# Kernel optimization log

Measured on AMD Instinct MI355X. Metric: run time of the kernel, lower is better.

## Reference

```python
import jax, jax.numpy as jnp
import numpy as np

N, E = 50000, 1600000
F_IN, EDGE_DIM, HID, HEADS, NCLS = 64, 16, 128, 4, 40
C = HID // HEADS  # per-head dim = 32


def setup_inputs() -> dict:
    key = jax.random.key(0)
    ks = jax.random.split(key, 20)
    s = 0.1
    inp = {
        'x': jax.random.normal(ks[0], (N, F_IN), jnp.float32),
        'edge_index': jax.random.randint(ks[1], (2, E), 0, N, jnp.int64),
        'edge_attr': jax.random.normal(ks[2], (E, EDGE_DIM), jnp.float32),
        # layer 1 params
        'W1': jax.random.normal(ks[3], (HID, F_IN), jnp.float32) * s,
        'as1': jax.random.normal(ks[4], (HEADS, C), jnp.float32) * s,
        'ad1': jax.random.normal(ks[5], (HEADS, C), jnp.float32) * s,
        'ae1': jax.random.normal(ks[6], (HEADS, C), jnp.float32) * s,
        'We1': jax.random.normal(ks[7], (HID, EDGE_DIM), jnp.float32) * s,
        'b1': jnp.zeros((HID,), jnp.float32),
        # layer 2 params
        'W2': jax.random.normal(ks[8], (HID, HID), jnp.float32) * s,
        'as2': jax.random.normal(ks[9], (HEADS, C), jnp.float32) * s,
        'ad2': jax.random.normal(ks[10], (HEADS, C), jnp.float32) * s,
        'ae2': jax.random.normal(ks[11], (HEADS, C), jnp.float32) * s,
        'We2': jax.random.normal(ks[12], (HID, EDGE_DIM), jnp.float32) * s,
        'b2': jnp.zeros((HID,), jnp.float32),
        # final classifier
        'Wlin': jax.random.normal(ks[13], (NCLS, HID), jnp.float32) * s,
        'blin': jnp.zeros((NCLS,), jnp.float32),
    }
    return inp


def gat_conv(x, src, dst, eattr, W, a_s, a_d, a_e, We, b):
    """PyG GATConv (concat=True, add_self_loops=True, fill_value='mean'), eval mode."""
    n = x.shape[0]
    H, Cd = a_s.shape
    h = (x @ W.T).reshape(n, H, Cd)  # [N,H,C]
    # self-loop edge_attr = per-destination mean of incoming edge_attr
    cnt = jax.ops.segment_sum(jnp.ones((dst.shape[0],), eattr.dtype), dst, num_segments=n)
    mean_ea = jax.ops.segment_sum(eattr, dst, num_segments=n) / jnp.maximum(cnt, 1.0)[:, None]
    loops = jnp.arange(n, dtype=src.dtype)
    s_idx = jnp.concatenate([src, loops])
    d_idx = jnp.concatenate([dst, loops])
    ea = jnp.concatenate([eattr, mean_ea], axis=0)  # [E+N, edge_dim]
    e = (ea @ We.T).reshape(-1, H, Cd)
    # edge-wise attention logits
    alpha = (h * a_s).sum(-1)[s_idx] + (h * a_d).sum(-1)[d_idx] + (e * a_e).sum(-1)  # [E+N,H]
    alpha = jax.nn.leaky_relu(alpha, 0.2)
    # segment softmax over destination neighborhoods (every node has a self-loop)
    amax = jax.ops.segment_max(alpha, d_idx, num_segments=n)
    ex = jnp.exp(alpha - amax[d_idx])
    den = jax.ops.segment_sum(ex, d_idx, num_segments=n)
    coef = ex / (den[d_idx] + 1e-16)
    out = jax.ops.segment_sum(h[s_idx] * coef[:, :, None], d_idx, num_segments=n)
    return out.reshape(n, H * Cd) + b


def reference(x, edge_index, edge_attr, W1, as1, ad1, ae1, We1, b1,
              W2, as2, ad2, ae2, We2, b2, Wlin, blin):
    src, dst = edge_index[0], edge_index[1]
    h = jax.nn.relu(gat_conv(x, src, dst, edge_attr, W1, as1, ad1, ae1, We1, b1))
    h = jax.nn.relu(gat_conv(h, src, dst, edge_attr, W2, as2, ad2, ae2, We2, b2))
    logits = h @ Wlin.T + blin
    return jax.nn.log_softmax(logits, axis=1)
```

## Files before the change

kernel.cpp:

```cpp
#include <hip/hip_runtime.h>
#include <hip/hip_bf16.h>
#include <math.h>


#define CHUNK 2048
#define CAPC 4608

typedef __attribute__((ext_vector_type(8))) short short8;
typedef __attribute__((ext_vector_type(4))) float floatx4;

__device__ __forceinline__ unsigned short f2bf(float f) {
  unsigned u = __float_as_uint(f);
  unsigned r = u + 0x7FFFu + ((u >> 16) & 1u);
  return (unsigned short)(r >> 16);
}
__device__ __forceinline__ float bf2f(unsigned short b) {
  return __uint_as_float(((unsigned)b) << 16);
}

__global__ __launch_bounds__(512) void hist_kernel(const int* __restrict__ dst,
                                                   int* __restrict__ bucketCnt,
                                                   int E, int NB) {
  __shared__ int hist[512];
  const int tid = threadIdx.x;
  hist[tid] = 0;
  __syncthreads();
  const int e0 = blockIdx.x * CHUNK, e1 = min(e0 + CHUNK, E);
  for (int e = e0 + tid; e < e1; e += 512) atomicAdd(&hist[dst[e] >> 7], 1);
  __syncthreads();
  if (tid < NB && hist[tid]) atomicAdd(&bucketCnt[tid], hist[tid]);
}

__global__ __launch_bounds__(512) void scanB_kernel(const int* __restrict__ bucketCnt,
                                                    int* __restrict__ bucketOffs,
                                                    int* __restrict__ bucketPos,
                                                    int* __restrict__ offs,
                                                    int NB, int N, int E) {
  __shared__ int sc[512];
  const int tid = threadIdx.x;
  const int v = (tid < NB) ? bucketCnt[tid] : 0;
  sc[tid] = v;
  __syncthreads();
  for (int off = 1; off < 512; off <<= 1) {
    int t = (tid >= off) ? sc[tid - off] : 0;
    __syncthreads();
    sc[tid] += t;
    __syncthreads();
  }
  const int excl = sc[tid] - v;
  if (tid < NB) { bucketOffs[tid] = excl; bucketPos[tid] = excl; }
  if (tid == 0) { bucketOffs[NB] = E; offs[N] = E; }
}

__global__ __launch_bounds__(512) void partB_kernel(const int* __restrict__ src,
                                                    const int* __restrict__ dst,
                                                    int* __restrict__ bucketPos,
                                                    int2* __restrict__ binned,
                                                    int E, int NB) {
  __shared__ int hist[512], sc[512], lbase[513], gbase[512], lcnt[512];
  __shared__ int2 stage[CHUNK];
  const int tid = threadIdx.x;
  const int e0 = blockIdx.x * CHUNK;
  const int e1 = min(e0 + CHUNK, E);
  hist[tid] = 0; lcnt[tid] = 0;
  __syncthreads();
  for (int e = e0 + tid; e < e1; e += 512) atomicAdd(&hist[dst[e] >> 7], 1);
  __syncthreads();
  sc[tid] = hist[tid];
  __syncthreads();
  for (int off = 1; off < 512; off <<= 1) {
    int t = (tid >= off) ? sc[tid - off] : 0;
    __syncthreads();
    sc[tid] += t;
    __syncthreads();
  }
  lbase[tid + 1] = sc[tid];
  if (tid == 0) lbase[0] = 0;
  if (tid < NB && hist[tid] > 0) gbase[tid] = atomicAdd(&bucketPos[tid], hist[tid]);
  __syncthreads();
  for (int e = e0 + tid; e < e1; e += 512) {
    const int d = dst[e];
    const int b = d >> 7;
    const int lr = atomicAdd(&lcnt[b], 1);
    int2 v;
    v.x = src[e];
    v.y = (int)(((unsigned)(d & 127) << 25) | (unsigned)e);
    stage[lbase[b] + lr] = v;
  }
  __syncthreads();
  const int total = e1 - e0;
  for (int t = tid; t < total; t += 512) {
    int lo = 0, hi = 511;
    while (lo < hi) {
      int mid = (lo + hi + 1) >> 1;
      if (lbase[mid] <= t) lo = mid; else hi = mid - 1;
    }
    binned[gbase[lo] + (t - lbase[lo])] = stage[t];
  }
}

__global__ __launch_bounds__(256) void passC_kernel(const int2* __restrict__ binned,
                                                    const int* __restrict__ bucketOffs,
                                                    int* __restrict__ srcS,
                                                    int* __restrict__ elist,
                                                    int* __restrict__ offs, int N) {
  __shared__ int cnt[128], dbase[129], dpos[128];
  __shared__ int2 stage[CAPC];
  const int tid = threadIdx.x;
  const int b = blockIdx.x;
  const int bo = bucketOffs[b], be = bucketOffs[b + 1];
  const int m = be - bo;
  if (tid < 128) { cnt[tid] = 0; dpos[tid] = 0; }
  __syncthreads();
  for (int t = tid; t < m; t += 256) {
    int2 v = binned[bo + t];
    if (t < CAPC) stage[t] = v;
    atomicAdd(&cnt[((unsigned)v.y) >> 25], 1);
  }
  __syncthreads();
  for (int off = 1; off < 128; off <<= 1) {
    int t = (tid < 128 && tid >= (unsigned)off) ? cnt[tid - off] : 0;
    __syncthreads();
    if (tid < 128) cnt[tid] += t;
    __syncthreads();
  }
  if (tid == 0) dbase[0] = 0;
  if (tid < 128) dbase[tid + 1] = cnt[tid];
  __syncthreads();
  const int dcnt = min(128, N - (b << 7));
  if (tid < dcnt) offs[(b << 7) + tid] = bo + dbase[tid];
  for (int t = tid; t < m; t += 256) {
    int2 v = (t < CAPC) ? stage[t] : binned[bo + t];
    const unsigned py = (unsigned)v.y;
    const int dl = py >> 25;
    const int p = dbase[dl] + atomicAdd(&dpos[dl], 1);
    srcS[bo + p] = v.x;
    elist[bo + p] = (int)(py & 0x1FFFFFFu);
  }
}

__global__ __launch_bounds__(128) void wa_kernel(const float* __restrict__ ae1,
                                                 const float* __restrict__ We1,
                                                 const float* __restrict__ ae2,
                                                 const float* __restrict__ We2,
                                                 float* __restrict__ Wa) {
  int t = threadIdx.x;
  const float* ae = (t < 64) ? ae1 : ae2;
  const float* We = (t < 64) ? We1 : We2;
  int h = (t >> 4) & 3;
  int d = t & 15;
  float s = 0.f;
  for (int c = 0; c < 32; ++c) s += ae[h * 32 + c] * We[(h * 32 + c) * 16 + d];
  Wa[t] = s;
}

__global__ __launch_bounds__(256) void cvt3_kernel(const float* __restrict__ a,
                                                   unsigned short* __restrict__ ao, int na,
                                                   const float* __restrict__ b,
                                                   unsigned short* __restrict__ bo, int nb,
                                                   const float* __restrict__ c,
                                                   unsigned short* __restrict__ co, int nc) {
  int i = blockIdx.x * 256 + threadIdx.x;
  if (i < na) ao[i] = f2bf(a[i]);
  else if (i < na + nb) bo[i - na] = f2bf(b[i - na]);
  else if (i < na + nb + nc) co[i - na - nb] = f2bf(c[i - na - nb]);
}

__global__ __launch_bounds__(256) void cvtw_kernel(const float* __restrict__ Wlin,
                                                   unsigned short* __restrict__ whi,
                                                   unsigned short* __restrict__ wlo) {
  int i = blockIdx.x * 256 + threadIdx.x;
  if (i >= 48 * 128) return;
  float v = (i < 40 * 128) ? Wlin[i] : 0.f;
  unsigned short h = f2bf(v);
  whi[i] = h;
  wlo[i] = f2bf(v - bf2f(h));
}

__global__ __launch_bounds__(256) void alphae12_kernel(const int* __restrict__ elist,
                                                       const float* __restrict__ ea,
                                                       const float* __restrict__ Wa,
                                                       unsigned short* __restrict__ ae1s,
                                                       unsigned short* __restrict__ ae2s,
                                                       int E) {
  __shared__ float wa[128];
  if (threadIdx.x < 128) wa[threadIdx.x] = Wa[threadIdx.x];
  __syncthreads();
  int j = blockIdx.x * 256 + threadIdx.x;
  if (j >= E) return;
  const int e = elist[j];
  const float4* p = (const float4*)(ea + (size_t)e * 16);
  float4 q0 = p[0], q1 = p[1], q2 = p[2], q3 = p[3];
  float v[16] = {q0.x, q0.y, q0.z, q0.w, q1.x, q1.y, q1.z, q1.w,
                 q2.x, q2.y, q2.z, q2.w, q3.x, q3.y, q3.z, q3.w};
  unsigned short rr[8];
#pragma unroll
  for (int h = 0; h < 8; ++h) {
    float s = 0.f;
#pragma unroll
    for (int d = 0; d < 16; ++d) s += v[d] * wa[h * 16 + d];
    rr[h] = f2bf(s);
  }
  ushort4 lo; lo.x = rr[0]; lo.y = rr[1]; lo.z = rr[2]; lo.w = rr[3];
  ushort4 hi; hi.x = rr[4]; hi.y = rr[5]; hi.z = rr[6]; hi.w = rr[7];
  *(ushort4*)(ae1s + (size_t)j * 4) = lo;
  *(ushort4*)(ae2s + (size_t)j * 4) = hi;
}

__global__ __launch_bounds__(256) void gemm_mfma_kernel(const unsigned short* __restrict__ X,
                                                        const unsigned short* __restrict__ Wb,
                                                        unsigned short* __restrict__ H,
                                                        int n, int K) {
  const int w = threadIdx.x >> 6;
  const int lane = threadIdx.x & 63;
  const int m0 = blockIdx.x * 64;
  const int quad = lane >> 4;
  const int l15 = lane & 15;
  floatx4 acc[4][2];
#pragma unroll
  for (int mt = 0; mt < 4; ++mt)
#pragma unroll
    for (int nt = 0; nt < 2; ++nt) acc[mt][nt] = (floatx4)(0.f);

  int rowm[4];
#pragma unroll
  for (int mt = 0; mt < 4; ++mt) {
    int r = m0 + mt * 16 + l15;
    rowm[mt] = (r < n) ? r : (n - 1);
  }
  const int ncol0 = (w << 5) + l15;

  for (int kc = 0; kc < K; kc += 32) {
    const int koff = kc + (quad << 3);
    short8 a[4], b[2];
#pragma unroll
    for (int mt = 0; mt < 4; ++mt)
      a[mt] = *(const short8*)(X + (size_t)rowm[mt] * K + koff);
#pragma unroll
    for (int nt = 0; nt < 2; ++nt)
      b[nt] = *(const short8*)(Wb + (size_t)(ncol0 + nt * 16) * K + koff);
#pragma unroll
    for (int mt = 0; mt < 4; ++mt)
#pragma unroll
      for (int nt = 0; nt < 2; ++nt)
        acc[mt][nt] = __builtin_amdgcn_mfma_f32_16x16x32_bf16(a[mt], b[nt], acc[mt][nt], 0, 0, 0);
  }
#pragma unroll
  for (int mt = 0; mt < 4; ++mt) {
    const int rbase = m0 + mt * 16 + (quad << 2);
#pragma unroll
    for (int nt = 0; nt < 2; ++nt) {
      const int col = ncol0 + nt * 16;
#pragma unroll
      for (int r = 0; r < 4; ++r) {
        const int row = rbase + r;
        if (row < n) H[(size_t)row * 128 + col] = f2bf(acc[mt][nt][r]);
      }
    }
  }
}

__global__ __launch_bounds__(256) void score_kernel(const unsigned short* __restrict__ h,
                                                    const float* __restrict__ a_s,
                                                    const float* __restrict__ a_d,
                                                    float* __restrict__ ssc,
                                                    float* __restrict__ dsc, int n) {
  int gid = blockIdx.x * 256 + threadIdx.x;
  int node = gid >> 6;
  int lane = threadIdx.x & 63;
  if (node >= n) return;
  int ch = lane * 2;
  ushort2 hq = *(const ushort2*)(h + (size_t)node * 128 + ch);
  float h0 = bf2f(hq.x), h1 = bf2f(hq.y);
  float ps = h0 * a_s[ch] + h1 * a_s[ch + 1];
  float pd = h0 * a_d[ch] + h1 * a_d[ch + 1];
#pragma unroll
  for (int off = 8; off; off >>= 1) {
    ps += __shfl_xor(ps, off, 16);
    pd += __shfl_xor(pd, off, 16);
  }
  if ((lane & 15) == 0) {
    int head = lane >> 4;
    ssc[node * 4 + head] = ps;
    dsc[node * 4 + head] = pd;
  }
}

__device__ __forceinline__ float leaky02(float a) { return a > 0.f ? a : 0.2f * a; }
__device__ __forceinline__ float sel4(float4 v, int h) {
  return (h == 0) ? v.x : (h == 1) ? v.y : (h == 2) ? v.z : v.w;
}

__global__ __launch_bounds__(256) void agg_kernel(const unsigned short* __restrict__ hin,
                                                  const float* __restrict__ ssc,
                                                  const float* __restrict__ dsc,
                                                  const unsigned short* __restrict__ aeS,
                                                  const int* __restrict__ offs,
                                                  const int* __restrict__ srcS,
                                                  const float* __restrict__ bias,
                                                  unsigned short* __restrict__ hout, int n) {
  __shared__ int sbuf[4][64];
  __shared__ float pbuf[4][256];
  const int tid = threadIdx.x;
  const int wv = tid >> 6;
  const int lane = tid & 63;
  const int node = blockIdx.x * 4 + wv;
  if (node >= n) return;
  const int l32 = lane & 31;
  const int half = lane >> 5;
  const int ch4 = l32 * 4;
  const int headB = l32 >> 3;
  const float4 dv = *(const float4*)(dsc + (size_t)node * 4);
  float4 l4 = make_float4(0.f, 0.f, 0.f, 0.f);
  float4 sa = make_float4(0.f, 0.f, 0.f, 0.f);
  float acc[4] = {0.f, 0.f, 0.f, 0.f};
  const int j0 = offs[node], j1 = offs[node + 1];

  for (int jc = j0; jc < j1; jc += 64) {
    const int len = min(64, j1 - jc);
    float4 p4 = make_float4(0.f, 0.f, 0.f, 0.f);
    int sv = 0;
    if (lane < len) {
      const int j = jc + lane;
      sv = srcS[j];
      const ushort4 aq = *(const ushort4*)(aeS + (size_t)j * 4);
      const float4 ae4 = make_float4(bf2f(aq.x), bf2f(aq.y), bf2f(aq.z), bf2f(aq.w));
      const float4 ss4 = *(const float4*)(ssc + (size_t)sv * 4);
      sa.x += ae4.x; sa.y += ae4.y; sa.z += ae4.z; sa.w += ae4.w;
      p4.x = __expf(leaky02(ss4.x + dv.x + ae4.x));
      p4.y = __expf(leaky02(ss4.y + dv.y + ae4.y));
      p4.z = __expf(leaky02(ss4.z + dv.z + ae4.z));
      p4.w = __expf(leaky02(ss4.w + dv.w + ae4.w));
    }
    sbuf[wv][lane] = sv;
    *(float4*)(&pbuf[wv][lane * 4]) = p4;
    l4.x += p4.x; l4.y += p4.y; l4.z += p4.z; l4.w += p4.w;
    int k = 0;
    for (; k + 8 <= len; k += 8) {
      int kk0 = k + half, kk1 = k + 2 + half, kk2 = k + 4 + half, kk3 = k + 6 + half;
      int s0 = sbuf[wv][kk0], s1 = sbuf[wv][kk1], s2 = sbuf[wv][kk2], s3 = sbuf[wv][kk3];
      float p0 = pbuf[wv][kk0 * 4 + headB], p1 = pbuf[wv][kk1 * 4 + headB];
      float p2 = pbuf[wv][kk2 * 4 + headB], p3 = pbuf[wv][kk3 * 4 + headB];
      uint2 d0 = *(const uint2*)(hin + (size_t)s0 * 128 + ch4);
      uint2 d1 = *(const uint2*)(hin + (size_t)s1 * 128 + ch4);
      uint2 d2 = *(const uint2*)(hin + (size_t)s2 * 128 + ch4);
      uint2 d3 = *(const uint2*)(hin + (size_t)s3 * 128 + ch4);
      acc[0] += p0 * __uint_as_float(d0.x << 16);
      acc[1] += p0 * __uint_as_float(d0.x & 0xFFFF0000u);
      acc[2] += p0 * __uint_as_float(d0.y << 16);
      acc[3] += p0 * __uint_as_float(d0.y & 0xFFFF0000u);
      acc[0] += p1 * __uint_as_float(d1.x << 16);
      acc[1] += p1 * __uint_as_float(d1.x & 0xFFFF0000u);
      acc[2] += p1 * __uint_as_float(d1.y << 16);
      acc[3] += p1 * __uint_as_float(d1.y & 0xFFFF0000u);
      acc[0] += p2 * __uint_as_float(d2.x << 16);
      acc[1] += p2 * __uint_as_float(d2.x & 0xFFFF0000u);
      acc[2] += p2 * __uint_as_float(d2.y << 16);
      acc[3] += p2 * __uint_as_float(d2.y & 0xFFFF0000u);
      acc[0] += p3 * __uint_as_float(d3.x << 16);
      acc[1] += p3 * __uint_as_float(d3.x & 0xFFFF0000u);
      acc[2] += p3 * __uint_as_float(d3.y << 16);
      acc[3] += p3 * __uint_as_float(d3.y & 0xFFFF0000u);
    }
    for (; k < len; k += 2) {
      int kk = k + half;
      if (kk < len) {
        int s = sbuf[wv][kk];
        float p = pbuf[wv][kk * 4 + headB];
        uint2 d = *(const uint2*)(hin + (size_t)s * 128 + ch4);
        acc[0] += p * __uint_as_float(d.x << 16);
        acc[1] += p * __uint_as_float(d.x & 0xFFFF0000u);
        acc[2] += p * __uint_as_float(d.y << 16);
        acc[3] += p * __uint_as_float(d.y & 0xFFFF0000u);
      }
    }
  }

#pragma unroll
  for (int off = 32; off; off >>= 1) {
    sa.x += __shfl_xor(sa.x, off);
    sa.y += __shfl_xor(sa.y, off);
    sa.z += __shfl_xor(sa.z, off);
    sa.w += __shfl_xor(sa.w, off);
    l4.x += __shfl_xor(l4.x, off);
    l4.y += __shfl_xor(l4.y, off);
    l4.z += __shfl_xor(l4.z, off);
    l4.w += __shfl_xor(l4.w, off);
  }
#pragma unroll
  for (int i = 0; i < 4; ++i) acc[i] += __shfl_xor(acc[i], 32);

  const int deg = j1 - j0;
  const float invd = 1.f / fmaxf((float)deg, 1.f);
  const float ssn = ssc[(size_t)node * 4 + headB];
  const float aloop = leaky02(ssn + sel4(dv, headB) + sel4(sa, headB) * invd);
  const float pl = __expf(aloop);
  const float lF = sel4(l4, headB) + pl;
  const uint2 hd = *(const uint2*)(hin + (size_t)node * 128 + ch4);
  const float hv0 = __uint_as_float(hd.x << 16);
  const float hv1 = __uint_as_float(hd.x & 0xFFFF0000u);
  const float hv2 = __uint_as_float(hd.y << 16);
  const float hv3 = __uint_as_float(hd.y & 0xFFFF0000u);
  const float inv = 1.f / (lF + 1e-16f);
  const float4 bi = *(const float4*)(bias + ch4);
  const float o0 = fmaxf((acc[0] + pl * hv0) * inv + bi.x, 0.f);
  const float o1 = fmaxf((acc[1] + pl * hv1) * inv + bi.y, 0.f);
  const float o2 = fmaxf((acc[2] + pl * hv2) * inv + bi.z, 0.f);
  const float o3 = fmaxf((acc[3] + pl * hv3) * inv + bi.w, 0.f);
  if (half == 0) {
    ushort4 o;
    o.x = f2bf(o0); o.y = f2bf(o1); o.z = f2bf(o2); o.w = f2bf(o3);
    *(ushort4*)(hout + (size_t)node * 128 + ch4) = o;
  }
}

__global__ __launch_bounds__(256) void classifier_kernel(const unsigned short* __restrict__ h,
                                                         const unsigned short* __restrict__ Whi,
                                                         const unsigned short* __restrict__ Wlo,
                                                         const float* __restrict__ blin,
                                                         float* __restrict__ out, int n) {
  const int w = threadIdx.x >> 6;
  const int lane = threadIdx.x & 63;
  const int quad = lane >> 4;
  const int l15 = lane & 15;
  const int row0 = blockIdx.x * 64 + w * 16;
  if (row0 >= n) return;
  int rowm = row0 + l15;
  if (rowm >= n) rowm = n - 1;
  floatx4 acc[3];
#pragma unroll
  for (int nt = 0; nt < 3; ++nt) acc[nt] = (floatx4)(0.f);
  const size_t hbase = (size_t)rowm * 128;
#pragma unroll
  for (int kc = 0; kc < 128; kc += 32) {
    const int koff = kc + (quad << 3);
    short8 a = *(const short8*)(h + hbase + koff);
#pragma unroll
    for (int nt = 0; nt < 3; ++nt) {
      short8 bh = *(const short8*)(Whi + (size_t)(nt * 16 + l15) * 128 + koff);
      short8 bl = *(const short8*)(Wlo + (size_t)(nt * 16 + l15) * 128 + koff);
      acc[nt] = __builtin_amdgcn_mfma_f32_16x16x32_bf16(a, bh, acc[nt], 0, 0, 0);
      acc[nt] = __builtin_amdgcn_mfma_f32_16x16x32_bf16(a, bl, acc[nt], 0, 0, 0);
    }
  }
  const float bl0 = blin[l15];
  const float bl1 = blin[16 + l15];
  const float bl2 = (l15 < 8) ? blin[32 + l15] : 0.f;
#pragma unroll
  for (int r = 0; r < 4; ++r) {
    const int rrow = row0 + (quad << 2) + r;
    const float v0 = acc[0][r] + bl0;
    const float v1 = acc[1][r] + bl1;
    const float v2 = (l15 < 8) ? (acc[2][r] + bl2) : -INFINITY;
    float m = fmaxf(v0, fmaxf(v1, v2));
#pragma unroll
    for (int off = 8; off; off >>= 1) m = fmaxf(m, __shfl_xor(m, off, 16));
    const float e2 = (l15 < 8) ? __expf(v2 - m) : 0.f;
    float s = __expf(v0 - m) + __expf(v1 - m) + e2;
#pragma unroll
    for (int off = 8; off; off >>= 1) s += __shfl_xor(s, off, 16);
    const float ls = m + __logf(s);
    if (rrow < n) {
      float* po = out + (size_t)rrow * 40;
      po[l15] = v0 - ls;
      po[16 + l15] = v1 - ls;
      if (l15 < 8) po[32 + l15] = v2 - ls;
    }
  }
}

extern "C" void kernel_launch(void* const* d_in, const int* in_sizes, int n_in,
                              void* d_out, int out_size, void* d_ws, size_t ws_size,
                              hipStream_t stream) {
  const float* x    = (const float*)d_in[0];
  const int*   eidx = (const int*)d_in[1];
  const float* ea   = (const float*)d_in[2];
  const float* W1   = (const float*)d_in[3];
  const float* as1  = (const float*)d_in[4];
  const float* ad1  = (const float*)d_in[5];
  const float* ae1w = (const float*)d_in[6];
  const float* We1  = (const float*)d_in[7];
  const float* b1   = (const float*)d_in[8];
  const float* W2   = (const float*)d_in[9];
  const float* as2  = (const float*)d_in[10];
  const float* ad2  = (const float*)d_in[11];
  const float* ae2w = (const float*)d_in[12];
  const float* We2  = (const float*)d_in[13];
  const float* b2   = (const float*)d_in[14];
  const float* Wlin = (const float*)d_in[15];
  const float* blin = (const float*)d_in[16];
  float* out = (float*)d_out;

  const int N = in_sizes[0] / 64;
  const int E = in_sizes[1] / 2;
  const int* src = eidx;
  const int* dst = eidx + E;
  const int NB = (N + 127) >> 7;

  char* wsb = (char*)d_ws;
  size_t off = 0;
  auto alloc = [&](size_t bytes) -> void* {
    void* p = wsb + off;
    off = (off + bytes + 255) & ~(size_t)255;
    return p;
  };
  int* bucketCnt  = (int*)alloc(512 * 4);
  int* bucketOffs = (int*)alloc(513 * 4);
  int* bucketPos  = (int*)alloc(512 * 4);
  int* offs       = (int*)alloc((size_t)(N + 1) * 4);
  void* bhA       = alloc((size_t)E * 8 > (size_t)N * 256 ? (size_t)E * 8 : (size_t)N * 256);
  int2* binned    = (int2*)bhA;
  unsigned short* hA = (unsigned short*)bhA;
  int* srcS       = (int*)alloc((size_t)E * 4);
  int* elist      = (int*)alloc((size_t)E * 4);
  float* Wa       = (float*)alloc(128 * 4);
  unsigned short* xb  = (unsigned short*)alloc((size_t)N * 64 * 2);
  unsigned short* Wb1 = (unsigned short*)alloc(128 * 64 * 2);
  unsigned short* Wb2 = (unsigned short*)alloc(128 * 128 * 2);
  unsigned short* Wlh = (unsigned short*)alloc(48 * 128 * 2);
  unsigned short* Wll = (unsigned short*)alloc(48 * 128 * 2);
  float* ssc      = (float*)alloc((size_t)N * 4 * 4);
  float* dsc      = (float*)alloc((size_t)N * 4 * 4);
  unsigned short* ae1s = (unsigned short*)alloc((size_t)E * 4 * 2);
  unsigned short* ae2s = (unsigned short*)alloc((size_t)E * 4 * 2);
  unsigned short* hB   = (unsigned short*)alloc((size_t)N * 128 * 2);

  const int ge = (E + 255) / 256;
  const int gg = (N + 63) / 64;
  const int gs = (N + 3) / 4;
  const int gp = (E + CHUNK - 1) / CHUNK;
  const int ncvt = N * 64 + 128 * 64 + 128 * 128;

  hipMemsetAsync(bucketCnt, 0, 512 * 4, stream);
  hist_kernel<<<gp, 512, 0, stream>>>(dst, bucketCnt, E, NB);
  scanB_kernel<<<1, 512, 0, stream>>>(bucketCnt, bucketOffs, bucketPos, offs, NB, N, E);
  partB_kernel<<<gp, 512, 0, stream>>>(src, dst, bucketPos, binned, E, NB);
  passC_kernel<<<NB, 256, 0, stream>>>(binned, bucketOffs, srcS, elist, offs, N);

  wa_kernel<<<1, 128, 0, stream>>>(ae1w, We1, ae2w, We2, Wa);
  cvt3_kernel<<<(ncvt + 255) / 256, 256, 0, stream>>>(x, xb, N * 64, W1, Wb1, 128 * 64,
                                                      W2, Wb2, 128 * 128);
  cvtw_kernel<<<24, 256, 0, stream>>>(Wlin, Wlh, Wll);
  alphae12_kernel<<<ge, 256, 0, stream>>>(elist, ea, Wa, ae1s, ae2s, E);

  gemm_mfma_kernel<<<gg, 256, 0, stream>>>(xb, Wb1, hA, N, 64);
  score_kernel<<<gs, 256, 0, stream>>>(hA, as1, ad1, ssc, dsc, N);
  agg_kernel<<<gs, 256, 0, stream>>>(hA, ssc, dsc, ae1s, offs, srcS, b1, hB, N);

  gemm_mfma_kernel<<<gg, 256, 0, stream>>>(hB, Wb2, hA, N, 128);
  score_kernel<<<gs, 256, 0, stream>>>(hA, as2, ad2, ssc, dsc, N);
  agg_kernel<<<gs, 256, 0, stream>>>(hA, ssc, dsc, ae2s, offs, srcS, b2, hB, N);

  classifier_kernel<<<gg, 256, 0, stream>>>(hB, Wlh, Wll, blin, out, N);
}
```

Baseline: 478.9 us.

## Replace two-pass bucket partition CSR build with atomic count-scan-scatter

Swaps the bucketed two-level partition sort (hist, bucket scan, partB, passC) for a per-node degree count with global atomics, a three-stage prefix scan, and an atomic-cursor scatter into CSR order. The edge-attention precompute now reads edge attributes sequentially and scatters its bf16 outputs to each edge's CSR position, rather than gathering through an edge list. This removes the staging buffers and binary searches but relies on heavy global atomics on random destinations. Order within each neighbourhood becomes nondeterministic, which may slightly change summation order and locality.

```diff
diff --git a/kernel.cpp b/kernel.cpp
--- a/kernel.cpp
+++ b/kernel.cpp
@@ -2,9 +2,6 @@
 #include <hip/hip_bf16.h>
 #include <math.h>
 
-
-#define CHUNK 2048
-#define CAPC 4608
 
 typedef __attribute__((ext_vector_type(8))) short short8;
 typedef __attribute__((ext_vector_type(4))) float floatx4;
@@ -18,125 +15,70 @@
   return __uint_as_float(((unsigned)b) << 16);
 }
 
-__global__ __launch_bounds__(512) void hist_kernel(const int* __restrict__ dst,
-                                                   int* __restrict__ bucketCnt,
-                                                   int E, int NB) {
-  __shared__ int hist[512];
+
+__global__ __launch_bounds__(256) void countN_kernel(const int* __restrict__ dst,
+                                                     int* __restrict__ cnt, int E) {
+  int i = blockIdx.x * 256 + threadIdx.x;
+  const int stride = gridDim.x * 256;
+  for (; i < E; i += stride) atomicAdd(&cnt[dst[i]], 1);
+}
+
+__global__ __launch_bounds__(256) void scanA_kernel(const int* __restrict__ cnt,
+                                                    int* __restrict__ offs,
+                                                    int* __restrict__ blockSum, int N) {
+  __shared__ int sc[256];
   const int tid = threadIdx.x;
-  hist[tid] = 0;
-  __syncthreads();
-  const int e0 = blockIdx.x * CHUNK, e1 = min(e0 + CHUNK, E);
-  for (int e = e0 + tid; e < e1; e += 512) atomicAdd(&hist[dst[e] >> 7], 1);
-  __syncthreads();
-  if (tid < NB && hist[tid]) atomicAdd(&bucketCnt[tid], hist[tid]);
-}
-
-__global__ __launch_bounds__(512) void scanB_kernel(const int* __restrict__ bucketCnt,
-                                                    int* __restrict__ bucketOffs,
-                                                    int* __restrict__ bucketPos,
-                                                    int* __restrict__ offs,
-                                                    int NB, int N, int E) {
-  __shared__ int sc[512];
-  const int tid = threadIdx.x;
-  const int v = (tid < NB) ? bucketCnt[tid] : 0;
+  const int i = blockIdx.x * 256 + tid;
+  const int v = (i < N) ? cnt[i] : 0;
   sc[tid] = v;
   __syncthreads();
-  for (int off = 1; off < 512; off <<= 1) {
+  for (int off = 1; off < 256; off <<= 1) {
     int t = (tid >= off) ? sc[tid - off] : 0;
     __syncthreads();
     sc[tid] += t;
     __syncthreads();
   }
-  const int excl = sc[tid] - v;
-  if (tid < NB) { bucketOffs[tid] = excl; bucketPos[tid] = excl; }
-  if (tid == 0) { bucketOffs[NB] = E; offs[N] = E; }
-}
-
-__global__ __launch_bounds__(512) void partB_kernel(const int* __restrict__ src,
-                                                    const int* __restrict__ dst,
-                                                    int* __restrict__ bucketPos,
-                                                    int2* __restrict__ binned,
-                                                    int E, int NB) {
-  __shared__ int hist[512], sc[512], lbase[513], gbase[512], lcnt[512];
-  __shared__ int2 stage[CHUNK];
+  if (i < N) offs[i] = sc[tid] - v;
+  if (tid == 255) blockSum[blockIdx.x] = sc[255];
+}
+
+__global__ __launch_bounds__(256) void scanBlk_kernel(int* __restrict__ blockSum, int NBLK) {
+  __shared__ int sc[256];
   const int tid = threadIdx.x;
-  const int e0 = blockIdx.x * CHUNK;
-  const int e1 = min(e0 + CHUNK, E);
-  hist[tid] = 0; lcnt[tid] = 0;
+  const int v = (tid < NBLK) ? blockSum[tid] : 0;
+  sc[tid] = v;
   __syncthreads();
-  for (int e = e0 + tid; e < e1; e += 512) atomicAdd(&hist[dst[e] >> 7], 1);
-  __syncthreads();
-  sc[tid] = hist[tid];
-  __syncthreads();
-  for (int off = 1; off < 512; off <<= 1) {
+  for (int off = 1; off < 256; off <<= 1) {
     int t = (tid >= off) ? sc[tid - off] : 0;
     __syncthreads();
     sc[tid] += t;
     __syncthreads();
   }
-  lbase[tid + 1] = sc[tid];
-  if (tid == 0) lbase[0] = 0;
-  if (tid < NB && hist[tid] > 0) gbase[tid] = atomicAdd(&bucketPos[tid], hist[tid]);
-  __syncthreads();
-  for (int e = e0 + tid; e < e1; e += 512) {
-    const int d = dst[e];
-    const int b = d >> 7;
-    const int lr = atomicAdd(&lcnt[b], 1);
-    int2 v;
-    v.x = src[e];
-    v.y = (int)(((unsigned)(d & 127) << 25) | (unsigned)e);
-    stage[lbase[b] + lr] = v;
-  }
-  __syncthreads();
-  const int total = e1 - e0;
-  for (int t = tid; t < total; t += 512) {
-    int lo = 0, hi = 511;
-    while (lo < hi) {
-      int mid = (lo + hi + 1) >> 1;
-      if (lbase[mid] <= t) lo = mid; else hi = mid - 1;
-    }
-    binned[gbase[lo] + (t - lbase[lo])] = stage[t];
-  }
-}
-
-__global__ __launch_bounds__(256) void passC_kernel(const int2* __restrict__ binned,
-                                                    const int* __restrict__ bucketOffs,
-                                                    int* __restrict__ srcS,
-                                                    int* __restrict__ elist,
-                                                    int* __restrict__ offs, int N) {
-  __shared__ int cnt[128], dbase[129], dpos[128];
-  __shared__ int2 stage[CAPC];
-  const int tid = threadIdx.x;
-  const int b = blockIdx.x;
-  const int bo = bucketOffs[b], be = bucketOffs[b + 1];
-  const int m = be - bo;
-  if (tid < 128) { cnt[tid] = 0; dpos[tid] = 0; }
-  __syncthreads();
-  for (int t = tid; t < m; t += 256) {
-    int2 v = binned[bo + t];
-    if (t < CAPC) stage[t] = v;
-    atomicAdd(&cnt[((unsigned)v.y) >> 25], 1);
-  }
-  __syncthreads();
-  for (int off = 1; off < 128; off <<= 1) {
-    int t = (tid < 128 && tid >= (unsigned)off) ? cnt[tid - off] : 0;
-    __syncthreads();
-    if (tid < 128) cnt[tid] += t;
-    __syncthreads();
-  }
-  if (tid == 0) dbase[0] = 0;
-  if (tid < 128) dbase[tid + 1] = cnt[tid];
-  __syncthreads();
-  const int dcnt = min(128, N - (b << 7));
-  if (tid < dcnt) offs[(b << 7) + tid] = bo + dbase[tid];
-  for (int t = tid; t < m; t += 256) {
-    int2 v = (t < CAPC) ? stage[t] : binned[bo + t];
-    const unsigned py = (unsigned)v.y;
-    const int dl = py >> 25;
-    const int p = dbase[dl] + atomicAdd(&dpos[dl], 1);
-    srcS[bo + p] = v.x;
-    elist[bo + p] = (int)(py & 0x1FFFFFFu);
-  }
+  if (tid < NBLK) blockSum[tid] = sc[tid] - v;
+}
+
+__global__ __launch_bounds__(256) void finz_kernel(int* __restrict__ offs,
+                                                   const int* __restrict__ blockSum,
+                                                   int* __restrict__ cursor, int N, int E) {
+  const int i = blockIdx.x * 256 + threadIdx.x;
+  if (i < N) {
+    const int v = offs[i] + blockSum[i >> 8];
+    offs[i] = v;
+    cursor[i] = v;
+  }
+  if (i == N) offs[N] = E;
+}
+
+__global__ __launch_bounds__(256) void scatter_kernel(const int* __restrict__ src,
+                                                      const int* __restrict__ dst,
+                                                      int* __restrict__ cursor,
+                                                      int* __restrict__ srcS,
+                                                      int* __restrict__ pos, int E) {
+  const int e = blockIdx.x * 256 + threadIdx.x;
+  if (e >= E) return;
+  const int p = atomicAdd(&cursor[dst[e]], 1);
+  srcS[p] = src[e];
+  pos[e] = p;
 }
 
 __global__ __launch_bounds__(128) void wa_kernel(const float* __restrict__ ae1,
@@ -177,7 +119,7 @@
   wlo[i] = f2bf(v - bf2f(h));
 }
 
-__global__ __launch_bounds__(256) void alphae12_kernel(const int* __restrict__ elist,
+__global__ __launch_bounds__(256) void alphae12_kernel(const int* __restrict__ pos,
                                                        const float* __restrict__ ea,
                                                        const float* __restrict__ Wa,
                                                        unsigned short* __restrict__ ae1s,
@@ -186,9 +128,8 @@
   __shared__ float wa[128];
   if (threadIdx.x < 128) wa[threadIdx.x] = Wa[threadIdx.x];
   __syncthreads();
-  int j = blockIdx.x * 256 + threadIdx.x;
-  if (j >= E) return;
-  const int e = elist[j];
+  int e = blockIdx.x * 256 + threadIdx.x;
+  if (e >= E) return;
   const float4* p = (const float4*)(ea + (size_t)e * 16);
   float4 q0 = p[0], q1 = p[1], q2 = p[2], q3 = p[3];
   float v[16] = {q0.x, q0.y, q0.z, q0.w, q1.x, q1.y, q1.z, q1.w,
@@ -203,8 +144,9 @@
   }
   ushort4 lo; lo.x = rr[0]; lo.y = rr[1]; lo.z = rr[2]; lo.w = rr[3];
   ushort4 hi; hi.x = rr[4]; hi.y = rr[5]; hi.z = rr[6]; hi.w = rr[7];
-  *(ushort4*)(ae1s + (size_t)j * 4) = lo;
-  *(ushort4*)(ae2s + (size_t)j * 4) = hi;
+  const int pp = pos[e];
+  *(ushort4*)(ae1s + (size_t)pp * 4) = lo;
+  *(ushort4*)(ae2s + (size_t)pp * 4) = hi;
 }
 
 __global__ __launch_bounds__(256) void gemm_mfma_kernel(const unsigned short* __restrict__ X,
@@ -495,7 +437,6 @@
   const int E = in_sizes[1] / 2;
   const int* src = eidx;
   const int* dst = eidx + E;
-  const int NB = (N + 127) >> 7;
 
   char* wsb = (char*)d_ws;
   size_t off = 0;
@@ -504,15 +445,13 @@
     off = (off + bytes + 255) & ~(size_t)255;
     return p;
   };
-  int* bucketCnt  = (int*)alloc(512 * 4);
-  int* bucketOffs = (int*)alloc(513 * 4);
-  int* bucketPos  = (int*)alloc(512 * 4);
+  int* cnt        = (int*)alloc((size_t)N * 4);
   int* offs       = (int*)alloc((size_t)(N + 1) * 4);
-  void* bhA       = alloc((size_t)E * 8 > (size_t)N * 256 ? (size_t)E * 8 : (size_t)N * 256);
-  int2* binned    = (int2*)bhA;
-  unsigned short* hA = (unsigned short*)bhA;
+  int* cursor     = (int*)alloc((size_t)N * 4);
+  int* blockSum   = (int*)alloc(256 * 4);
+  unsigned short* hA = (unsigned short*)alloc((size_t)N * 256);
   int* srcS       = (int*)alloc((size_t)E * 4);
-  int* elist      = (int*)alloc((size_t)E * 4);
+  int* pos        = (int*)alloc((size_t)E * 4);
   float* Wa       = (float*)alloc(128 * 4);
   unsigned short* xb  = (unsigned short*)alloc((size_t)N * 64 * 2);
   unsigned short* Wb1 = (unsigned short*)alloc(128 * 64 * 2);
@@ -528,20 +467,21 @@
   const int ge = (E + 255) / 256;
   const int gg = (N + 63) / 64;
   const int gs = (N + 3) / 4;
-  const int gp = (E + CHUNK - 1) / CHUNK;
+  const int NBLK = (N + 255) / 256;
   const int ncvt = N * 64 + 128 * 64 + 128 * 128;
 
-  hipMemsetAsync(bucketCnt, 0, 512 * 4, stream);
-  hist_kernel<<<gp, 512, 0, stream>>>(dst, bucketCnt, E, NB);
-  scanB_kernel<<<1, 512, 0, stream>>>(bucketCnt, bucketOffs, bucketPos, offs, NB, N, E);
-  partB_kernel<<<gp, 512, 0, stream>>>(src, dst, bucketPos, binned, E, NB);
-  passC_kernel<<<NB, 256, 0, stream>>>(binned, bucketOffs, srcS, elist, offs, N);
+  hipMemsetAsync(cnt, 0, (size_t)N * 4, stream);
+  countN_kernel<<<2048, 256, 0, stream>>>(dst, cnt, E);
+  scanA_kernel<<<NBLK, 256, 0, stream>>>(cnt, offs, blockSum, N);
+  scanBlk_kernel<<<1, 256, 0, stream>>>(blockSum, NBLK);
+  finz_kernel<<<(N + 256) / 256 + 1, 256, 0, stream>>>(offs, blockSum, cursor, N, E);
+  scatter_kernel<<<ge, 256, 0, stream>>>(src, dst, cursor, srcS, pos, E);
 
   wa_kernel<<<1, 128, 0, stream>>>(ae1w, We1, ae2w, We2, Wa);
   cvt3_kernel<<<(ncvt + 255) / 256, 256, 0, stream>>>(x, xb, N * 64, W1, Wb1, 128 * 64,
                                                       W2, Wb2, 128 * 128);
   cvtw_kernel<<<24, 256, 0, stream>>>(Wlin, Wlh, Wll);
-  alphae12_kernel<<<ge, 256, 0, stream>>>(elist, ea, Wa, ae1s, ae2s, E);
+  alphae12_kernel<<<ge, 256, 0, stream>>>(pos, ea, Wa, ae1s, ae2s, E);
 
   gemm_mfma_kernel<<<gg, 256, 0, stream>>>(xb, Wb1, hA, N, 64);
   score_kernel<<<gs, 256, 0, stream>>>(hA, as1, ad1, ssc, dsc, N);
```

After: 632.8 us. +32.2%, slower.

## Compute edge attention terms in edge order and carry them through the sort

Applied to the files above, without the earlier changes.

Edge-attribute attention projections are now computed in original edge order, so the edge_attr reads are contiguous. The results travel as payload through the two-pass bucket partition, which makes the elist index array and the scattered gather of edge_attr rows unnecessary. Source indices are packed into 16 bits next to the local destination, which assumes N fits in 16 bits. The cost is wider records in the partition passes (20 bytes per edge instead of 8) and extra intermediate traffic, plus aliasing of scratch buffers.

```diff
diff --git a/kernel.cpp b/kernel.cpp
--- a/kernel.cpp
+++ b/kernel.cpp
@@ -4,7 +4,6 @@
 
 
 #define CHUNK 2048
-#define CAPC 4608
 
 typedef __attribute__((ext_vector_type(8))) short short8;
 typedef __attribute__((ext_vector_type(4))) float floatx4;
@@ -16,127 +15,6 @@
 }
 __device__ __forceinline__ float bf2f(unsigned short b) {
   return __uint_as_float(((unsigned)b) << 16);
-}
-
-__global__ __launch_bounds__(512) void hist_kernel(const int* __restrict__ dst,
-                                                   int* __restrict__ bucketCnt,
-                                                   int E, int NB) {
-  __shared__ int hist[512];
-  const int tid = threadIdx.x;
-  hist[tid] = 0;
-  __syncthreads();
-  const int e0 = blockIdx.x * CHUNK, e1 = min(e0 + CHUNK, E);
-  for (int e = e0 + tid; e < e1; e += 512) atomicAdd(&hist[dst[e] >> 7], 1);
-  __syncthreads();
-  if (tid < NB && hist[tid]) atomicAdd(&bucketCnt[tid], hist[tid]);
-}
-
-__global__ __launch_bounds__(512) void scanB_kernel(const int* __restrict__ bucketCnt,
-                                                    int* __restrict__ bucketOffs,
-                                                    int* __restrict__ bucketPos,
-                                                    int* __restrict__ offs,
-                                                    int NB, int N, int E) {
-  __shared__ int sc[512];
-  const int tid = threadIdx.x;
-  const int v = (tid < NB) ? bucketCnt[tid] : 0;
-  sc[tid] = v;
-  __syncthreads();
-  for (int off = 1; off < 512; off <<= 1) {
-    int t = (tid >= off) ? sc[tid - off] : 0;
-    __syncthreads();
-    sc[tid] += t;
-    __syncthreads();
-  }
-  const int excl = sc[tid] - v;
-  if (tid < NB) { bucketOffs[tid] = excl; bucketPos[tid] = excl; }
-  if (tid == 0) { bucketOffs[NB] = E; offs[N] = E; }
-}
-
-__global__ __launch_bounds__(512) void partB_kernel(const int* __restrict__ src,
-                                                    const int* __restrict__ dst,
-                                                    int* __restrict__ bucketPos,
-                                                    int2* __restrict__ binned,
-                                                    int E, int NB) {
-  __shared__ int hist[512], sc[512], lbase[513], gbase[512], lcnt[512];
-  __shared__ int2 stage[CHUNK];
-  const int tid = threadIdx.x;
-  const int e0 = blockIdx.x * CHUNK;
-  const int e1 = min(e0 + CHUNK, E);
-  hist[tid] = 0; lcnt[tid] = 0;
-  __syncthreads();
-  for (int e = e0 + tid; e < e1; e += 512) atomicAdd(&hist[dst[e] >> 7], 1);
-  __syncthreads();
-  sc[tid] = hist[tid];
-  __syncthreads();
-  for (int off = 1; off < 512; off <<= 1) {
-    int t = (tid >= off) ? sc[tid - off] : 0;
-    __syncthreads();
-    sc[tid] += t;
-    __syncthreads();
-  }
-  lbase[tid + 1] = sc[tid];
-  if (tid == 0) lbase[0] = 0;
-  if (tid < NB && hist[tid] > 0) gbase[tid] = atomicAdd(&bucketPos[tid], hist[tid]);
-  __syncthreads();
-  for (int e = e0 + tid; e < e1; e += 512) {
-    const int d = dst[e];
-    const int b = d >> 7;
-    const int lr = atomicAdd(&lcnt[b], 1);
-    int2 v;
-    v.x = src[e];
-    v.y = (int)(((unsigned)(d & 127) << 25) | (unsigned)e);
-    stage[lbase[b] + lr] = v;
-  }
-  __syncthreads();
-  const int total = e1 - e0;
-  for (int t = tid; t < total; t += 512) {
-    int lo = 0, hi = 511;
-    while (lo < hi) {
-      int mid = (lo + hi + 1) >> 1;
-      if (lbase[mid] <= t) lo = mid; else hi = mid - 1;
-    }
-    binned[gbase[lo] + (t - lbase[lo])] = stage[t];
-  }
-}
-
-__global__ __launch_bounds__(256) void passC_kernel(const int2* __restrict__ binned,
-                                                    const int* __restrict__ bucketOffs,
-                                                    int* __restrict__ srcS,
-                                                    int* __restrict__ elist,
-                                                    int* __restrict__ offs, int N) {
-  __shared__ int cnt[128], dbase[129], dpos[128];
-  __shared__ int2 stage[CAPC];
-  const int tid = threadIdx.x;
-  const int b = blockIdx.x;
-  const int bo = bucketOffs[b], be = bucketOffs[b + 1];
-  const int m = be - bo;
-  if (tid < 128) { cnt[tid] = 0; dpos[tid] = 0; }
-  __syncthreads();
-  for (int t = tid; t < m; t += 256) {
-    int2 v = binned[bo + t];
-    if (t < CAPC) stage[t] = v;
-    atomicAdd(&cnt[((unsigned)v.y) >> 25], 1);
-  }
-  __syncthreads();
-  for (int off = 1; off < 128; off <<= 1) {
-    int t = (tid < 128 && tid >= (unsigned)off) ? cnt[tid - off] : 0;
-    __syncthreads();
-    if (tid < 128) cnt[tid] += t;
-    __syncthreads();
-  }
-  if (tid == 0) dbase[0] = 0;
-  if (tid < 128) dbase[tid + 1] = cnt[tid];
-  __syncthreads();
-  const int dcnt = min(128, N - (b << 7));
-  if (tid < dcnt) offs[(b << 7) + tid] = bo + dbase[tid];
-  for (int t = tid; t < m; t += 256) {
-    int2 v = (t < CAPC) ? stage[t] : binned[bo + t];
-    const unsigned py = (unsigned)v.y;
-    const int dl = py >> 25;
-    const int p = dbase[dl] + atomicAdd(&dpos[dl], 1);
-    srcS[bo + p] = v.x;
-    elist[bo + p] = (int)(py & 0x1FFFFFFu);
-  }
 }
 
 __global__ __launch_bounds__(128) void wa_kernel(const float* __restrict__ ae1,
@@ -154,6 +32,170 @@
   Wa[t] = s;
 }
 
+__global__ __launch_bounds__(256) void alphaseq_kernel(const float* __restrict__ ea,
+                                                       const float* __restrict__ Wa,
+                                                       uint2* __restrict__ tA1,
+                                                       uint2* __restrict__ tA2, int E) {
+  __shared__ float wa[128];
+  if (threadIdx.x < 128) wa[threadIdx.x] = Wa[threadIdx.x];
+  __syncthreads();
+  int e = blockIdx.x * 256 + threadIdx.x;
+  if (e >= E) return;
+  const float4* p = (const float4*)(ea + (size_t)e * 16);
+  float4 q0 = p[0], q1 = p[1], q2 = p[2], q3 = p[3];
+  float v[16] = {q0.x, q0.y, q0.z, q0.w, q1.x, q1.y, q1.z, q1.w,
+                 q2.x, q2.y, q2.z, q2.w, q3.x, q3.y, q3.z, q3.w};
+  unsigned short rr[8];
+#pragma unroll
+  for (int h = 0; h < 8; ++h) {
+    float s = 0.f;
+#pragma unroll
+    for (int d = 0; d < 16; ++d) s += v[d] * wa[h * 16 + d];
+    rr[h] = f2bf(s);
+  }
+  uint2 lo, hi;
+  lo.x = ((unsigned)rr[1] << 16) | rr[0];
+  lo.y = ((unsigned)rr[3] << 16) | rr[2];
+  hi.x = ((unsigned)rr[5] << 16) | rr[4];
+  hi.y = ((unsigned)rr[7] << 16) | rr[6];
+  tA1[e] = lo;
+  tA2[e] = hi;
+}
+
+__global__ __launch_bounds__(512) void hist_kernel(const int* __restrict__ dst,
+                                                   int* __restrict__ bucketCnt,
+                                                   int E, int NB) {
+  __shared__ int hist[512];
+  const int tid = threadIdx.x;
+  hist[tid] = 0;
+  __syncthreads();
+  const int e0 = blockIdx.x * CHUNK, e1 = min(e0 + CHUNK, E);
+  for (int e = e0 + tid; e < e1; e += 512) atomicAdd(&hist[dst[e] >> 7], 1);
+  __syncthreads();
+  if (tid < NB && hist[tid]) atomicAdd(&bucketCnt[tid], hist[tid]);
+}
+
+__global__ __launch_bounds__(512) void scanB_kernel(const int* __restrict__ bucketCnt,
+                                                    int* __restrict__ bucketOffs,
+                                                    int* __restrict__ bucketPos,
+                                                    int* __restrict__ offs,
+                                                    int NB, int N, int E) {
+  __shared__ int sc[512];
+  const int tid = threadIdx.x;
+  const int v = (tid < NB) ? bucketCnt[tid] : 0;
+  sc[tid] = v;
+  __syncthreads();
+  for (int off = 1; off < 512; off <<= 1) {
+    int t = (tid >= off) ? sc[tid - off] : 0;
+    __syncthreads();
+    sc[tid] += t;
+    __syncthreads();
+  }
+  const int excl = sc[tid] - v;
+  if (tid < NB) { bucketOffs[tid] = excl; bucketPos[tid] = excl; }
+  if (tid == 0) { bucketOffs[NB] = E; offs[N] = E; }
+}
+
+__global__ __launch_bounds__(512) void partB_kernel(const int* __restrict__ src,
+                                                    const int* __restrict__ dst,
+                                                    const uint2* __restrict__ tA1,
+                                                    const uint2* __restrict__ tA2,
+                                                    int* __restrict__ bucketPos,
+                                                    int4* __restrict__ binned16,
+                                                    int* __restrict__ binned4,
+                                                    int E, int NB) {
+  __shared__ int hist[512], sc[512], lbase[513], gbase[512], lcnt[512];
+  __shared__ int4 stg16[CHUNK];
+  __shared__ int stg4[CHUNK];
+  const int tid = threadIdx.x;
+  const int e0 = blockIdx.x * CHUNK;
+  const int e1 = min(e0 + CHUNK, E);
+  hist[tid] = 0; lcnt[tid] = 0;
+  __syncthreads();
+  for (int e = e0 + tid; e < e1; e += 512) atomicAdd(&hist[dst[e] >> 7], 1);
+  __syncthreads();
+  sc[tid] = hist[tid];
+  __syncthreads();
+  for (int off = 1; off < 512; off <<= 1) {
+    int t = (tid >= off) ? sc[tid - off] : 0;
+    __syncthreads();
+    sc[tid] += t;
+    __syncthreads();
+  }
+  lbase[tid + 1] = sc[tid];
+  if (tid == 0) lbase[0] = 0;
+  if (tid < NB && hist[tid] > 0) gbase[tid] = atomicAdd(&bucketPos[tid], hist[tid]);
+  __syncthreads();
+  for (int e = e0 + tid; e < e1; e += 512) {
+    const int d = dst[e];
+    const int b = d >> 7;
+    const int lr = atomicAdd(&lcnt[b], 1);
+    const uint2 a1 = tA1[e];
+    const uint2 a2 = tA2[e];
+    int4 v;
+    v.x = (src[e] & 0xFFFF) | ((d & 127) << 16);
+    v.y = (int)a1.x;
+    v.z = (int)a1.y;
+    v.w = (int)a2.x;
+    const int sp = lbase[b] + lr;
+    stg16[sp] = v;
+    stg4[sp] = (int)a2.y;
+  }
+  __syncthreads();
+  const int total = e1 - e0;
+  for (int t = tid; t < total; t += 512) {
+    int lo = 0, hi = 511;
+    while (lo < hi) {
+      int mid = (lo + hi + 1) >> 1;
+      if (lbase[mid] <= t) lo = mid; else hi = mid - 1;
+    }
+    const int g = gbase[lo] + (t - lbase[lo]);
+    binned16[g] = stg16[t];
+    binned4[g] = stg4[t];
+  }
+}
+
+__global__ __launch_bounds__(256) void passC_kernel(const int4* __restrict__ binned16,
+                                                    const int* __restrict__ binned4,
+                                                    const int* __restrict__ bucketOffs,
+                                                    int* __restrict__ srcS,
+                                                    uint2* __restrict__ aeS1,
+                                                    uint2* __restrict__ aeS2,
+                                                    int* __restrict__ offs, int N) {
+  __shared__ int cnt[128], dbase[129], dpos[128];
+  const int tid = threadIdx.x;
+  const int b = blockIdx.x;
+  const int bo = bucketOffs[b], be = bucketOffs[b + 1];
+  const int m = be - bo;
+  if (tid < 128) { cnt[tid] = 0; dpos[tid] = 0; }
+  __syncthreads();
+  for (int t = tid; t < m; t += 256) {
+    const int4 v = binned16[bo + t];
+    atomicAdd(&cnt[(v.x >> 16) & 127], 1);
+  }
+  __syncthreads();
+  for (int off = 1; off < 128; off <<= 1) {
+    int t = (tid < 128 && tid >= (unsigned)off) ? cnt[tid - off] : 0;
+    __syncthreads();
+    if (tid < 128) cnt[tid] += t;
+    __syncthreads();
+  }
+  if (tid == 0) dbase[0] = 0;
+  if (tid < 128) dbase[tid + 1] = cnt[tid];
+  __syncthreads();
+  const int dcnt = min(128, N - (b << 7));
+  if (tid < dcnt) offs[(b << 7) + tid] = bo + dbase[tid];
+  for (int t = tid; t < m; t += 256) {
+    const int4 v = binned16[bo + t];
+    const int w4 = binned4[bo + t];
+    const int dl = (v.x >> 16) & 127;
+    const int p = dbase[dl] + atomicAdd(&dpos[dl], 1);
+    srcS[bo + p] = v.x & 0xFFFF;
+    aeS1[bo + p] = make_uint2((unsigned)v.y, (unsigned)v.z);
+    aeS2[bo + p] = make_uint2((unsigned)v.w, (unsigned)w4);
+  }
+}
+
 __global__ __launch_bounds__(256) void cvt3_kernel(const float* __restrict__ a,
                                                    unsigned short* __restrict__ ao, int na,
                                                    const float* __restrict__ b,
@@ -175,36 +217,6 @@
   unsigned short h = f2bf(v);
   whi[i] = h;
   wlo[i] = f2bf(v - bf2f(h));
-}
-
-__global__ __launch_bounds__(256) void alphae12_kernel(const int* __restrict__ elist,
-                                                       const float* __restrict__ ea,
-                                                       const float* __restrict__ Wa,
-                                                       unsigned short* __restrict__ ae1s,
-                                                       unsigned short* __restrict__ ae2s,
-                                                       int E) {
-  __shared__ float wa[128];
-  if (threadIdx.x < 128) wa[threadIdx.x] = Wa[threadIdx.x];
-  __syncthreads();
-  int j = blockIdx.x * 256 + threadIdx.x;
-  if (j >= E) return;
-  const int e = elist[j];
-  const float4* p = (const float4*)(ea + (size_t)e * 16);
-  float4 q0 = p[0], q1 = p[1], q2 = p[2], q3 = p[3];
-  float v[16] = {q0.x, q0.y, q0.z, q0.w, q1.x, q1.y, q1.z, q1.w,
-                 q2.x, q2.y, q2.z, q2.w, q3.x, q3.y, q3.z, q3.w};
-  unsigned short rr[8];
-#pragma unroll
-  for (int h = 0; h < 8; ++h) {
-    float s = 0.f;
-#pragma unroll
-    for (int d = 0; d < 16; ++d) s += v[d] * wa[h * 16 + d];
-    rr[h] = f2bf(s);
-  }
-  ushort4 lo; lo.x = rr[0]; lo.y = rr[1]; lo.z = rr[2]; lo.w = rr[3];
-  ushort4 hi; hi.x = rr[4]; hi.y = rr[5]; hi.z = rr[6]; hi.w = rr[7];
-  *(ushort4*)(ae1s + (size_t)j * 4) = lo;
-  *(ushort4*)(ae2s + (size_t)j * 4) = hi;
 }
 
 __global__ __launch_bounds__(256) void gemm_mfma_kernel(const unsigned short* __restrict__ X,
@@ -508,22 +520,25 @@
   int* bucketOffs = (int*)alloc(513 * 4);
   int* bucketPos  = (int*)alloc(512 * 4);
   int* offs       = (int*)alloc((size_t)(N + 1) * 4);
-  void* bhA       = alloc((size_t)E * 8 > (size_t)N * 256 ? (size_t)E * 8 : (size_t)N * 256);
-  int2* binned    = (int2*)bhA;
-  unsigned short* hA = (unsigned short*)bhA;
+  uint2* tA1      = (uint2*)alloc((size_t)E * 8);
+  uint2* tA2      = (uint2*)alloc((size_t)E * 8);
+  void* regC      = alloc((size_t)E * 16);
+  int4* binned16  = (int4*)regC;
+  unsigned short* hA = (unsigned short*)regC;
+  void* regD      = alloc((size_t)E * 4);
+  int* binned4    = (int*)regD;
+  unsigned short* xb = (unsigned short*)regD;
   int* srcS       = (int*)alloc((size_t)E * 4);
-  int* elist      = (int*)alloc((size_t)E * 4);
   float* Wa       = (float*)alloc(128 * 4);
-  unsigned short* xb  = (unsigned short*)alloc((size_t)N * 64 * 2);
   unsigned short* Wb1 = (unsigned short*)alloc(128 * 64 * 2);
   unsigned short* Wb2 = (unsigned short*)alloc(128 * 128 * 2);
   unsigned short* Wlh = (unsigned short*)alloc(48 * 128 * 2);
   unsigned short* Wll = (unsigned short*)alloc(48 * 128 * 2);
   float* ssc      = (float*)alloc((size_t)N * 4 * 4);
   float* dsc      = (float*)alloc((size_t)N * 4 * 4);
-  unsigned short* ae1s = (unsigned short*)alloc((size_t)E * 4 * 2);
-  unsigned short* ae2s = (unsigned short*)alloc((size_t)E * 4 * 2);
-  unsigned short* hB   = (unsigned short*)alloc((size_t)N * 128 * 2);
+  unsigned short* hB = (unsigned short*)alloc((size_t)N * 128 * 2);
+  uint2* aeS1 = tA1;
+  uint2* aeS2 = tA2;
 
   const int ge = (E + 255) / 256;
   const int gg = (N + 63) / 64;
@@ -532,24 +547,24 @@
   const int ncvt = N * 64 + 128 * 64 + 128 * 128;
 
   hipMemsetAsync(bucketCnt, 0, 512 * 4, stream);
+  wa_kernel<<<1, 128, 0, stream>>>(ae1w, We1, ae2w, We2, Wa);
+  alphaseq_kernel<<<ge, 256, 0, stream>>>(ea, Wa, tA1, tA2, E);
   hist_kernel<<<gp, 512, 0, stream>>>(dst, bucketCnt, E, NB);
   scanB_kernel<<<1, 512, 0, stream>>>(bucketCnt, bucketOffs, bucketPos, offs, NB, N, E);
-  partB_kernel<<<gp, 512, 0, stream>>>(src, dst, bucketPos, binned, E, NB);
-  passC_kernel<<<NB, 256, 0, stream>>>(binned, bucketOffs, srcS, elist, offs, N);
-
-  wa_kernel<<<1, 128, 0, stream>>>(ae1w, We1, ae2w, We2, Wa);
+  partB_kernel<<<gp, 512, 0, stream>>>(src, dst, tA1, tA2, bucketPos, binned16, binned4, E, NB);
+  passC_kernel<<<NB, 256, 0, stream>>>(binned16, binned4, bucketOffs, srcS, aeS1, aeS2, offs, N);
+
   cvt3_kernel<<<(ncvt + 255) / 256, 256, 0, stream>>>(x, xb, N * 64, W1, Wb1, 128 * 64,
                                                       W2, Wb2, 128 * 128);
   cvtw_kernel<<<24, 256, 0, stream>>>(Wlin, Wlh, Wll);
-  alphae12_kernel<<<ge, 256, 0, stream>>>(elist, ea, Wa, ae1s, ae2s, E);
 
   gemm_mfma_kernel<<<gg, 256, 0, stream>>>(xb, Wb1, hA, N, 64);
   score_kernel<<<gs, 256, 0, stream>>>(hA, as1, ad1, ssc, dsc, N);
-  agg_kernel<<<gs, 256, 0, stream>>>(hA, ssc, dsc, ae1s, offs, srcS, b1, hB, N);
+  agg_kernel<<<gs, 256, 0, stream>>>(hA, ssc, dsc, (const unsigned short*)aeS1, offs, srcS, b1, hB, N);
 
   gemm_mfma_kernel<<<gg, 256, 0, stream>>>(hB, Wb2, hA, N, 128);
   score_kernel<<<gs, 256, 0, stream>>>(hA, as2, ad2, ssc, dsc, N);
-  agg_kernel<<<gs, 256, 0, stream>>>(hA, ssc, dsc, ae2s, offs, srcS, b2, hB, N);
+  agg_kernel<<<gs, 256, 0, stream>>>(hA, ssc, dsc, (const unsigned short*)aeS2, offs, srcS, b2, hB, N);
 
   classifier_kernel<<<gg, 256, 0, stream>>>(hB, Wlh, Wll, blin, out, N);
 }
```

Result: slower. 490.6 us (+2.5%).
